# Kernel optimization log

Hardware: AMD Instinct MI355X
Metric: run time of the kernel (lower is better)

Reference implementation:

```python
import jax, jax.numpy as jnp
import numpy as np

LK = 8  # db4 has 8 taps
LEVEL = 5
# pywt.Wavelet('db4').filter_bank[0] == dec_lo
DB4_LO = np.array([-0.010597401784997278, 0.032883011666982945, 0.030841381835986965,
                   -0.18703481171888114, -0.02798376941698385, 0.6308807679295904,
                   0.7148465705525415, 0.23037781330885523], dtype=np.float32)
DN = ('NCH', 'OIH', 'NCH')


def _wpt_kernels(level):
    # Filter_Free WPT: distinct kernel per child node; parent j even -> (lp, hp), odd -> (hp, lp)
    cmf = (-1.0) ** np.arange(LK)
    k_lp = DB4_LO
    k_hp = (DB4_LO[::-1] * cmf).astype(np.float32)
    ks = []
    for i in range(level):
        rows = []
        for j in range(2 ** i):
            rows += [k_lp, k_hp] if j % 2 == 0 else [k_hp, k_lp]
        ks.append(jnp.asarray(np.stack(rows)))  # [2^(i+1), LK]
    return ks


def setup_inputs() -> dict:
    key = jax.random.key(0)
    kx, kb = jax.random.split(key)
    B, N = 128, 32768
    inp = {'x': jax.random.normal(kx, (B, 1, N), dtype=jnp.float32)}
    for i, K in enumerate(_wpt_kernels(LEVEL)):
        inp[f'k{i + 1}'] = K
    for i in range(LEVEL):
        kb, sub = jax.random.split(kb)
        # small positive thresholds (Act_Init=0 would make the threshold an exact identity)
        inp[f'b{i + 1}'] = 0.1 * jax.random.uniform(sub, (2 ** (i + 1),), dtype=jnp.float32)
    return inp


def _analysis(c, K, b):
    # c: [B, G, M] parents -> [B, 2G, M//2] children; one grouped 8-tap conv for the whole level
    G = c.shape[1]
    cp = jnp.pad(c, ((0, 0), (0, 0), (LK // 2 - 1, LK // 2)))
    y = jax.lax.conv_general_dilated(cp, K[:, None, :], (2,), 'VALID',
                                     feature_group_count=G, dimension_numbers=DN)
    bb = b[None, :, None]
    # symmetric sigmoid soft-threshold (Thresh_SigSym), fused elementwise
    return y * (jax.nn.sigmoid(10.0 * (y - bb)) + jax.nn.sigmoid(-10.0 * (y + bb)))


def _synthesis(y, K):
    # adjoint of the strided analysis conv (conv_transpose): [B, 2G, M] -> [B, G, 2M]
    G = y.shape[1] // 2
    M = y.shape[2]
    W = jnp.flip(K, -1).reshape(G, 2, LK)  # sum the two children of each parent
    out = jax.lax.conv_general_dilated(y, W, (1,), [(LK - 1, LK - 1)], lhs_dilation=(2,),
                                       feature_group_count=G, dimension_numbers=DN)
    pl = LK // 2 - 1  # undo analysis left pad
    return out[:, :, pl:pl + 2 * M]


def reference(x, k1, k2, k3, k4, k5, b1, b2, b3, b4, b5):
    Ks = [k1, k2, k3, k4, k5]
    bs = [b1, b2, b3, b4, b5]
    c = x  # [B, 1, N]
    for K, b in zip(Ks, bs):
        c = _analysis(c, K, b)
    for K in Ks[::-1]:
        c = _synthesis(c, K)
    return c  # [B, 1, N] reconstruction
```

## Files before the change

### kernel.cpp

```cpp
#include <hip/hip_runtime.h>

#define TPB 256

constexpr int NSEQ = 32768;
constexpr int C0   = 2048;


__device__ __forceinline__ float gate(float y, float bb) {
    float e1 = __expf(-10.f * (y - bb));
    float e2 = __expf( 10.f * (y + bb));
    return __builtin_amdgcn_rcpf(1.f + e1) + __builtin_amdgcn_rcpf(1.f + e2);
}

template<int Lin, int Lout, int Gout, int Nlev>
__device__ __forceinline__ void analysis_step(
    const float* __restrict__ in, float* __restrict__ out,
    const float* __restrict__ kf, const float* __restrict__ bias, int outBase)
{
    constexpr int TOT = Lout * Gout;
    for (int idx = threadIdx.x; idx < TOT; idx += TPB) {
        const int ch = idx / Lout;
        const int i  = idx - ch * Lout;
        const float* __restrict__ krow = kf + ch * 8;
        const float* __restrict__ ip   = in + (ch >> 1) * Lin + 2 * i;
        float y = 0.f;
#pragma unroll
        for (int t = 0; t < 8; ++t) y = fmaf(ip[t], krow[t], y);
        const int m = outBase + i;
        const float v = y * gate(y, bias[ch]);
        out[idx] = ((unsigned)m < (unsigned)Nlev) ? v : 0.f;
    }
}

template<int Lin, int Lout, int Gout, int Nlev>
__device__ __forceinline__ void synth_step(
    const float* __restrict__ in, float* __restrict__ out,
    const float* __restrict__ kf, int outBase)
{
    constexpr int TOT = Lout * Gout;
    for (int idx = threadIdx.x; idx < TOT; idx += TPB) {
        const int g  = idx / Lout;
        const int nl = idx - g * Lout;
        const float* __restrict__ y0 = in + (2 * g) * Lin;
        const float* __restrict__ y1 = y0 + Lin;
        const float* __restrict__ k0 = kf + (2 * g) * 8;
        const float* __restrict__ k1 = k0 + 8;
        const int j0 = (nl + 1) >> 1;
        const int kb = 7 - (nl & 1);
        float acc = 0.f;
#pragma unroll
        for (int q = 0; q < 4; ++q) {
            acc = fmaf(y0[j0 + q], k0[kb - 2 * q], acc);
            acc = fmaf(y1[j0 + q], k1[kb - 2 * q], acc);
        }
        const int n = outBase + nl;
        out[idx] = ((unsigned)n < (unsigned)Nlev) ? acc : 0.f;
    }
}

__global__ __launch_bounds__(TPB) void wpt_fused(
    const float* __restrict__ x,
    const float* __restrict__ K1, const float* __restrict__ K2,
    const float* __restrict__ K3, const float* __restrict__ K4,
    const float* __restrict__ K5,
    const float* __restrict__ B1, const float* __restrict__ B2,
    const float* __restrict__ B3, const float* __restrict__ B4,
    const float* __restrict__ B5,
    float* __restrict__ out)
{
    __shared__ float bufA[2496];
    __shared__ float bufB[2496];
    __shared__ float kf[496];
    __shared__ float bss[62];

    const int tid   = threadIdx.x;
    const int batch = blockIdx.x >> 4;
    const int cid   = blockIdx.x & 15;
    const int s     = cid * C0;

    {
        const float* kin[5] = {K1, K2, K3, K4, K5};
        const float* bin[5] = {B1, B2, B3, B4, B5};
        const int koff[5] = {0, 16, 48, 112, 240};
        const int boff[5] = {0, 2, 6, 14, 30};
#pragma unroll
        for (int l = 0; l < 5; ++l) {
            for (int i = tid; i < (16 << l); i += TPB) kf[koff[l] + i] = kin[l][i];
            for (int i = tid; i < (2  << l); i += TPB) bss[boff[l] + i] = bin[l][i];
        }
    }

    {
        const float* xb = x + batch * NSEQ;
        const int base = s - 221;
        for (int i = tid; i < 2490; i += TPB) {
            const int g = base + i;
            bufA[i] = ((unsigned)g < (unsigned)NSEQ) ? xb[g] : 0.f;
        }
    }
    __syncthreads();

    analysis_step<2490, 1242,  2, 16384>(bufA, bufB, kf + 0,   bss + 0,  (s >> 1) - 109);
    __syncthreads();
    analysis_step<1242,  618,  4,  8192>(bufB, bufA, kf + 16,  bss + 2,  (s >> 2) - 53);
    __syncthreads();
    analysis_step< 618,  306,  8,  4096>(bufA, bufB, kf + 48,  bss + 6,  (s >> 3) - 25);
    __syncthreads();
    analysis_step< 306,  150, 16,  2048>(bufB, bufA, kf + 112, bss + 14, (s >> 4) - 11);
    __syncthreads();
    analysis_step< 150,   72, 32,  1024>(bufA, bufB, kf + 240, bss + 30, (s >> 5) - 4);
    __syncthreads();

    synth_step<  72,  136, 16,  2048>(bufB, bufA, kf + 240, (s >> 4) - 4);
    __syncthreads();
    synth_step< 136,  264,  8,  4096>(bufA, bufB, kf + 112, (s >> 3) - 4);
    __syncthreads();
    synth_step< 264,  520,  4,  8192>(bufB, bufA, kf + 48,  (s >> 2) - 4);
    __syncthreads();
    synth_step< 520, 1032,  2, 16384>(bufA, bufB, kf + 16,  (s >> 1) - 4);
    __syncthreads();

    {
        float* ob = out + batch * NSEQ + s;
        const float* __restrict__ y0 = bufB;
        const float* __restrict__ y1 = bufB + 1032;
        for (int i = tid; i < C0; i += TPB) {
            const int nl = i + 4;
            const int j0 = (nl + 1) >> 1;
            const int kb = 7 - (nl & 1);
            float acc = 0.f;
#pragma unroll
            for (int q = 0; q < 4; ++q) {
                acc = fmaf(y0[j0 + q], kf[kb - 2 * q],     acc);
                acc = fmaf(y1[j0 + q], kf[8 + kb - 2 * q], acc);
            }
            ob[i] = acc;
        }
    }
}

extern "C" void kernel_launch(void* const* d_in, const int* in_sizes, int n_in,
                              void* d_out, int out_size, void* d_ws, size_t ws_size,
                              hipStream_t stream) {
    const int nbatch = in_sizes[0] / NSEQ;
    wpt_fused<<<dim3(nbatch * (NSEQ / C0)), dim3(TPB), 0, stream>>>(
        (const float*)d_in[0],
        (const float*)d_in[1], (const float*)d_in[2],
        (const float*)d_in[3], (const float*)d_in[4],
        (const float*)d_in[5],
        (const float*)d_in[6], (const float*)d_in[7],
        (const float*)d_in[8], (const float*)d_in[9],
        (const float*)d_in[10],
        (float*)d_out);
}
```

Baseline: 134.2 us.

## Register-block WPT stages with float4 LDS access and sibling-channel reuse

Each analysis step now has a thread compute 4 outputs for both children of one parent from a single 16-float window, and each synthesis step computes 8 outputs per thread. LDS reads and writes become float4, and the buffers are padded and aligned to strides that are multiples of 4. This cuts LDS traffic, integer index math and redundant input loads per output. In exchange it raises register pressure and computes some padded outputs that are not needed.

```diff
diff --git a/kernel.cpp b/kernel.cpp
--- a/kernel.cpp
+++ b/kernel.cpp
@@ -12,49 +12,101 @@
     return __builtin_amdgcn_rcpf(1.f + e1) + __builtin_amdgcn_rcpf(1.f + e2);
 }
 
-template<int Lin, int Lout, int Gout, int Nlev>
-__device__ __forceinline__ void analysis_step(
+template<int Sin, int Sout, int P, int Gout, int Nlev>
+__device__ __forceinline__ void analysis_r4(
     const float* __restrict__ in, float* __restrict__ out,
     const float* __restrict__ kf, const float* __restrict__ bias, int outBase)
 {
-    constexpr int TOT = Lout * Gout;
-    for (int idx = threadIdx.x; idx < TOT; idx += TPB) {
-        const int ch = idx / Lout;
-        const int i  = idx - ch * Lout;
-        const float* __restrict__ krow = kf + ch * 8;
-        const float* __restrict__ ip   = in + (ch >> 1) * Lin + 2 * i;
-        float y = 0.f;
-#pragma unroll
-        for (int t = 0; t < 8; ++t) y = fmaf(ip[t], krow[t], y);
-        const int m = outBase + i;
-        const float v = y * gate(y, bias[ch]);
-        out[idx] = ((unsigned)m < (unsigned)Nlev) ? v : 0.f;
-    }
-}
-
-template<int Lin, int Lout, int Gout, int Nlev>
-__device__ __forceinline__ void synth_step(
+    constexpr int TPC = P / 4;
+    constexpr int TOT = (Gout / 2) * TPC;
+    for (int task = threadIdx.x; task < TOT; task += TPB) {
+        const int c  = task / TPC;
+        const int i0 = (task - c * TPC) * 4;
+
+        float w[16];
+        {
+            const float4* ip = reinterpret_cast<const float4*>(in + c * Sin + 2 * i0);
+            reinterpret_cast<float4*>(w)[0] = ip[0];
+            reinterpret_cast<float4*>(w)[1] = ip[1];
+            reinterpret_cast<float4*>(w)[2] = ip[2];
+            reinterpret_cast<float4*>(w)[3] = ip[3];
+        }
+        float k0[8], k1[8];
+        {
+            const float4* kp = reinterpret_cast<const float4*>(kf + (2 * c) * 8);
+            reinterpret_cast<float4*>(k0)[0] = kp[0];
+            reinterpret_cast<float4*>(k0)[1] = kp[1];
+            reinterpret_cast<float4*>(k1)[0] = kp[2];
+            reinterpret_cast<float4*>(k1)[1] = kp[3];
+        }
+        const float b0 = bias[2 * c];
+        const float b1 = bias[2 * c + 1];
+
+        float o0[4], o1[4];
+#pragma unroll
+        for (int r = 0; r < 4; ++r) {
+            float ya = 0.f, yb = 0.f;
+#pragma unroll
+            for (int t = 0; t < 8; ++t) {
+                ya = fmaf(w[2 * r + t], k0[t], ya);
+                yb = fmaf(w[2 * r + t], k1[t], yb);
+            }
+            const int m = outBase + i0 + r;
+            const bool ok = ((unsigned)m < (unsigned)Nlev);
+            o0[r] = ok ? ya * gate(ya, b0) : 0.f;
+            o1[r] = ok ? yb * gate(yb, b1) : 0.f;
+        }
+        *reinterpret_cast<float4*>(out + (2 * c)     * Sout + i0) = *reinterpret_cast<float4*>(o0);
+        *reinterpret_cast<float4*>(out + (2 * c + 1) * Sout + i0) = *reinterpret_cast<float4*>(o1);
+    }
+}
+
+template<int Sin, int Sout, int P, int Gout, int Nlev>
+__device__ __forceinline__ void synth_r8(
     const float* __restrict__ in, float* __restrict__ out,
     const float* __restrict__ kf, int outBase)
 {
-    constexpr int TOT = Lout * Gout;
-    for (int idx = threadIdx.x; idx < TOT; idx += TPB) {
-        const int g  = idx / Lout;
-        const int nl = idx - g * Lout;
-        const float* __restrict__ y0 = in + (2 * g) * Lin;
-        const float* __restrict__ y1 = y0 + Lin;
-        const float* __restrict__ k0 = kf + (2 * g) * 8;
-        const float* __restrict__ k1 = k0 + 8;
-        const int j0 = (nl + 1) >> 1;
-        const int kb = 7 - (nl & 1);
-        float acc = 0.f;
-#pragma unroll
-        for (int q = 0; q < 4; ++q) {
-            acc = fmaf(y0[j0 + q], k0[kb - 2 * q], acc);
-            acc = fmaf(y1[j0 + q], k1[kb - 2 * q], acc);
-        }
-        const int n = outBase + nl;
-        out[idx] = ((unsigned)n < (unsigned)Nlev) ? acc : 0.f;
+    constexpr int TPG = P / 8;
+    constexpr int TOT = Gout * TPG;
+    for (int task = threadIdx.x; task < TOT; task += TPB) {
+        const int g   = task / TPG;
+        const int nl0 = (task - g * TPG) * 8;
+
+        float ya[8], yb[8];
+        {
+            const float4* p0 = reinterpret_cast<const float4*>(in + (2 * g) * Sin + nl0 / 2);
+            const float4* p1 = reinterpret_cast<const float4*>(in + (2 * g + 1) * Sin + nl0 / 2);
+            reinterpret_cast<float4*>(ya)[0] = p0[0];
+            reinterpret_cast<float4*>(ya)[1] = p0[1];
+            reinterpret_cast<float4*>(yb)[0] = p1[0];
+            reinterpret_cast<float4*>(yb)[1] = p1[1];
+        }
+        float k0[8], k1[8];
+        {
+            const float4* kp = reinterpret_cast<const float4*>(kf + (2 * g) * 8);
+            reinterpret_cast<float4*>(k0)[0] = kp[0];
+            reinterpret_cast<float4*>(k0)[1] = kp[1];
+            reinterpret_cast<float4*>(k1)[0] = kp[2];
+            reinterpret_cast<float4*>(k1)[1] = kp[3];
+        }
+
+        float o[8];
+#pragma unroll
+        for (int r = 0; r < 8; ++r) {
+            const int jr = (r + 1) >> 1;
+            const int kb = 7 - (r & 1);
+            float acc = 0.f;
+#pragma unroll
+            for (int q = 0; q < 4; ++q) {
+                acc = fmaf(ya[jr + q], k0[kb - 2 * q], acc);
+                acc = fmaf(yb[jr + q], k1[kb - 2 * q], acc);
+            }
+            const int m = outBase + nl0 + r;
+            o[r] = ((unsigned)m < (unsigned)Nlev) ? acc : 0.f;
+        }
+        float* op = out + g * Sout + nl0;
+        *reinterpret_cast<float4*>(op)     = *reinterpret_cast<float4*>(o);
+        *reinterpret_cast<float4*>(op + 4) = *reinterpret_cast<float4*>(o + 4);
     }
 }
 
@@ -68,9 +120,9 @@
     const float* __restrict__ B5,
     float* __restrict__ out)
 {
-    __shared__ float bufA[2496];
-    __shared__ float bufB[2496];
-    __shared__ float kf[496];
+    __shared__ __align__(16) float bufA[2528];
+    __shared__ __align__(16) float bufB[2512];
+    __shared__ __align__(16) float kf[496];
     __shared__ float bss[62];
 
     const int tid   = threadIdx.x;
@@ -93,49 +145,70 @@
     {
         const float* xb = x + batch * NSEQ;
         const int base = s - 221;
-        for (int i = tid; i < 2490; i += TPB) {
+        for (int i = tid; i < 2504; i += TPB) {
             const int g = base + i;
-            bufA[i] = ((unsigned)g < (unsigned)NSEQ) ? xb[g] : 0.f;
-        }
-    }
-    __syncthreads();
-
-    analysis_step<2490, 1242,  2, 16384>(bufA, bufB, kf + 0,   bss + 0,  (s >> 1) - 109);
-    __syncthreads();
-    analysis_step<1242,  618,  4,  8192>(bufB, bufA, kf + 16,  bss + 2,  (s >> 2) - 53);
-    __syncthreads();
-    analysis_step< 618,  306,  8,  4096>(bufA, bufB, kf + 48,  bss + 6,  (s >> 3) - 25);
-    __syncthreads();
-    analysis_step< 306,  150, 16,  2048>(bufB, bufA, kf + 112, bss + 14, (s >> 4) - 11);
-    __syncthreads();
-    analysis_step< 150,   72, 32,  1024>(bufA, bufB, kf + 240, bss + 30, (s >> 5) - 4);
-    __syncthreads();
-
-    synth_step<  72,  136, 16,  2048>(bufB, bufA, kf + 240, (s >> 4) - 4);
-    __syncthreads();
-    synth_step< 136,  264,  8,  4096>(bufA, bufB, kf + 112, (s >> 3) - 4);
-    __syncthreads();
-    synth_step< 264,  520,  4,  8192>(bufB, bufA, kf + 48,  (s >> 2) - 4);
-    __syncthreads();
-    synth_step< 520, 1032,  2, 16384>(bufA, bufB, kf + 16,  (s >> 1) - 4);
+            bufA[i] = (i < 2490 && (unsigned)g < (unsigned)NSEQ) ? xb[g] : 0.f;
+        }
+    }
+    __syncthreads();
+
+    analysis_r4<2504, 1256, 1248,  2, 16384>(bufA, bufB, kf + 0,   bss + 0,  (s >> 1) - 109);
+    __syncthreads();
+    analysis_r4<1256,  632,  624,  4,  8192>(bufB, bufA, kf + 16,  bss + 2,  (s >> 2) - 53);
+    __syncthreads();
+    analysis_r4< 632,  312,  312,  8,  4096>(bufA, bufB, kf + 48,  bss + 6,  (s >> 3) - 25);
+    __syncthreads();
+    analysis_r4< 312,  152,  152, 16,  2048>(bufB, bufA, kf + 112, bss + 14, (s >> 4) - 11);
+    __syncthreads();
+    analysis_r4< 152,   72,   72, 32,  1024>(bufA, bufB, kf + 240, bss + 30, (s >> 5) - 4);
+    __syncthreads();
+
+    synth_r8<  72,  136,  136, 16,  2048>(bufB, bufA, kf + 240, (s >> 4) - 4);
+    __syncthreads();
+    synth_r8< 136,  264,  264,  8,  4096>(bufA, bufB, kf + 112, (s >> 3) - 4);
+    __syncthreads();
+    synth_r8< 264,  520,  520,  4,  8192>(bufB, bufA, kf + 48,  (s >> 2) - 4);
+    __syncthreads();
+    synth_r8< 520, 1032, 1032,  2, 16384>(bufA, bufB, kf + 16,  (s >> 1) - 4);
     __syncthreads();
 
     {
         float* ob = out + batch * NSEQ + s;
-        const float* __restrict__ y0 = bufB;
-        const float* __restrict__ y1 = bufB + 1032;
-        for (int i = tid; i < C0; i += TPB) {
-            const int nl = i + 4;
-            const int j0 = (nl + 1) >> 1;
-            const int kb = 7 - (nl & 1);
+        const int i0 = tid * 8;
+        float ya[12], yb[12];
+        {
+            const float4* p0 = reinterpret_cast<const float4*>(bufB + i0 / 2);
+            const float4* p1 = reinterpret_cast<const float4*>(bufB + 1032 + i0 / 2);
+            reinterpret_cast<float4*>(ya)[0] = p0[0];
+            reinterpret_cast<float4*>(ya)[1] = p0[1];
+            reinterpret_cast<float4*>(ya)[2] = p0[2];
+            reinterpret_cast<float4*>(yb)[0] = p1[0];
+            reinterpret_cast<float4*>(yb)[1] = p1[1];
+            reinterpret_cast<float4*>(yb)[2] = p1[2];
+        }
+        float k0[8], k1[8];
+        {
+            const float4* kp = reinterpret_cast<const float4*>(kf);
+            reinterpret_cast<float4*>(k0)[0] = kp[0];
+            reinterpret_cast<float4*>(k0)[1] = kp[1];
+            reinterpret_cast<float4*>(k1)[0] = kp[2];
+            reinterpret_cast<float4*>(k1)[1] = kp[3];
+        }
+        float o[8];
+#pragma unroll
+        for (int r = 0; r < 8; ++r) {
+            const int jr = ((r + 1) >> 1) + 2;
+            const int kb = 7 - (r & 1);
             float acc = 0.f;
 #pragma unroll
             for (int q = 0; q < 4; ++q) {
-                acc = fmaf(y0[j0 + q], kf[kb - 2 * q],     acc);
-                acc = fmaf(y1[j0 + q], kf[8 + kb - 2 * q], acc);
+                acc = fmaf(ya[jr + q], k0[kb - 2 * q], acc);
+                acc = fmaf(yb[jr + q], k1[kb - 2 * q], acc);
             }
-            ob[i] = acc;
-        }
+            o[r] = acc;
+        }
+        *reinterpret_cast<float4*>(ob + i0)     = *reinterpret_cast<float4*>(o);
+        *reinterpret_cast<float4*>(ob + i0 + 4) = *reinterpret_cast<float4*>(o + 4);
     }
 }
 
```

After: 128.3 us. -4.4%, faster.
